# Optimization experiments

Measured on AMD Instinct MI355X. Metric: run time of the kernel, lower is better.

Reference implementation:

```python
import jax, jax.numpy as jnp
import numpy as np

EPS = 1e-7
N_INST = 16  # instance ids 1..16 (id 0 = background); all present w.h.p. given input distribution


def setup_inputs() -> dict:
    key = jax.random.key(0)
    k1, k2, k3 = jax.random.split(key, 3)
    pred_instance_mask = jax.random.uniform(k1, (4, 17, 768, 768), dtype=jnp.float32)
    cls_out = jax.random.uniform(k2, (4, 1, 768, 768), dtype=jnp.float32)
    target_mask = jax.random.randint(k3, (4, 1, 768, 768), 0, 17, dtype=jnp.int32)
    return {"pred_instance_mask": pred_instance_mask, "cls_out": cls_out, "target_mask": target_mask}


def _bce_dice(p, t):
    # BCEDiceLoss(activation=None): mean BCE on probabilities + soft-dice loss
    pc = jnp.clip(p, EPS, 1.0 - EPS)
    bce = -jnp.mean(t * jnp.log(pc) + (1.0 - t) * jnp.log1p(-pc))
    inter = jnp.sum(p * t)
    dice = 1.0 - (2.0 * inter + EPS) / (jnp.sum(p) + jnp.sum(t) + EPS)
    return bce + dice


def reference(pred_instance_mask, cls_out, target_mask):
    B, K, H, W = pred_instance_mask.shape
    tfg = (target_mask > 0).astype(jnp.float32)
    res = _bce_dice(cls_out, tfg)
    res = res + _bce_dice(pred_instance_mask[:, 0:1], 1.0 - tfg)

    # ---- pairwise BCEDice loss matrix L[n, k] for ids n=1..N_INST, channels k=1..K-1 ----
    # Each pairwise loss is over the FULL tensor (all B*H*W pixels), target = (target_mask == n).
    Pm = pred_instance_mask[:, 1:].transpose(1, 0, 2, 3).reshape(K - 1, -1)  # [K-1, M]
    Mpix = Pm.shape[1]
    tm = target_mask.reshape(-1)  # [M] int ids
    pc = jnp.clip(Pm, EPS, 1.0 - EPS)
    log1mp = jnp.log1p(-pc)
    D = log1mp - jnp.log(pc)  # [K-1, M]; BCE = mean(-log1mp) + mean(t * D)
    A = -jnp.mean(log1mp, axis=1)  # [K-1]
    segD = jax.ops.segment_sum(D.T, tm, num_segments=N_INST + 1)[1:]   # [N, K-1]
    segP = jax.ops.segment_sum(Pm.T, tm, num_segments=N_INST + 1)[1:]  # [N, K-1] = inter
    cnt = jax.ops.segment_sum(jnp.ones_like(tm, dtype=jnp.float32), tm, num_segments=N_INST + 1)[1:]  # [N]
    sum_p = jnp.sum(Pm, axis=1)  # [K-1]
    bce = A[None, :] + segD / jnp.float32(Mpix)
    dice = 1.0 - (2.0 * segP + EPS) / (sum_p[None, :] + cnt[:, None] + EPS)
    L = bce + dice  # [N, K-1]

    # ---- greedy assignment: ids in ascending order each grab the remaining best channel ----
    def step(carry, Ln):
        avail, total = carry
        masked = jnp.where(avail, Ln, jnp.inf)
        k = jnp.argmin(masked)
        return (avail.at[k].set(False), total + masked[k]), None

    (_, total), _ = jax.lax.scan(step, (jnp.ones(K - 1, dtype=bool), jnp.float32(0.0)), L)
    return (res + total) / N_INST
```

## Files before the change

### kernel.cpp

```cpp
#include <hip/hip_runtime.h>
#include <hip/hip_bf16.h>

#define HWPX 589824
#define MPIX 2359296
#define EPSF 1e-7f
#define LN2F 0.6931471805599453f
#define PXB  2304
#define NBLK 1024
#define MSTEPS 9


typedef __attribute__((ext_vector_type(8))) short bf16x8;
typedef __attribute__((ext_vector_type(4))) float f32x4;

__device__ __forceinline__ short bfc(float x) {
    union { __hip_bfloat16 h; short s; } u;
    u.h = __float2bfloat16(x);
    return u.s;
}

__device__ __forceinline__ float wave_sum64(float v) {
#pragma unroll
    for (int o = 32; o; o >>= 1) v += __shfl_xor(v, o, 64);
    return v;
}

__global__ __launch_bounds__(512, 8) void loss_main(
    const float* __restrict__ pred, const float* __restrict__ cls,
    const int* __restrict__ tm, float* __restrict__ acc)
{
    __shared__ float sD[8][256];
    __shared__ float sP[8][256];
    __shared__ float sCh[3][16][8];
    __shared__ float sC6[6][8];

    const int tid  = threadIdx.x;
    const int w    = tid >> 6;
    const int lane = tid & 63;
    const int g    = lane >> 4;
    const int q    = lane & 15;

    const long base = (long)blockIdx.x * PXB;
    const int b   = (int)(base / HWPX);
    const int off = (int)(base % HWPX);

    const int*   trow = tm   + (long)b * HWPX + off;
    const float* prow = pred + ((long)b * 17 + 1 + q) * (long)HWPX + off;

    f32x4 aD = {0.f, 0.f, 0.f, 0.f};
    f32x4 aP = {0.f, 0.f, 0.f, 0.f};
    float sl2 = 0.f, sp = 0.f, cf = 0.f;
    const int tgt = q + 1;
    const int lbase = w * 32 + g * 8;

#pragma unroll
    for (int s = 0; s < MSTEPS; ++s) {
        const int pxl = lbase + s * 256;
        const float4 pa = *(const float4*)(prow + pxl);
        const float4 pb = *(const float4*)(prow + pxl + 4);
        const int4   ta = *(const int4*)(trow + pxl);
        const int4   tb = *(const int4*)(trow + pxl + 4);
        const float pv[8] = {pa.x,pa.y,pa.z,pa.w,pb.x,pb.y,pb.z,pb.w};
        const int   tv[8] = {ta.x,ta.y,ta.z,ta.w,tb.x,tb.y,tb.z,tb.w};
        bf16x8 av, bD, bP;
#pragma unroll
        for (int j = 0; j < 8; ++j) {
            const float p  = pv[j];
            const float pc = fminf(fmaxf(p, EPSF), 1.0f - EPSF);
            const float l2p  = __log2f(pc);
            const float l21p = __log2f(1.0f - pc);
            sl2 += l21p;
            sp  += p;
            bD[j] = bfc(l21p - l2p);
            bP[j] = bfc(p);
            const bool m = (tv[j] == tgt);
            av[j] = m ? (short)0x3F80 : (short)0;
            cf += m ? 1.f : 0.f;
        }
        aD = __builtin_amdgcn_mfma_f32_16x16x32_bf16(av, bD, aD, 0, 0, 0);
        aP = __builtin_amdgcn_mfma_f32_16x16x32_bf16(av, bP, aP, 0, 0, 0);
    }

    sl2 += __shfl_xor(sl2, 16, 64); sl2 += __shfl_xor(sl2, 32, 64);
    sp  += __shfl_xor(sp,  16, 64); sp  += __shfl_xor(sp,  32, 64);
    cf  += __shfl_xor(cf,  16, 64); cf  += __shfl_xor(cf,  32, 64);
    if (lane < 16) { sCh[0][q][w] = sl2; sCh[1][q][w] = sp; sCh[2][q][w] = cf; }

    *(f32x4*)&sD[w][lane * 4] = aD;
    *(f32x4*)&sP[w][lane * 4] = aP;

    const float* crow = cls  + (long)b * HWPX + off;
    const float* zrow = pred + (long)b * 17 * (long)HWPX + off;
    float s0c=0.f,s1c=0.f,s2c=0.f, s00=0.f,s10=0.f,s20=0.f;
    const int nch = (tid < 64) ? 2 : 1;
    for (int chunk = 0; chunk < nch; ++chunk) {
        const int pbase = (chunk == 0) ? tid * 4 : 2048 + tid * 4;
        const float4 ca = *(const float4*)(crow + pbase);
        const float4 za = *(const float4*)(zrow + pbase);
        const int4   ua = *(const int4*)(trow + pbase);
        const float cv[4] = {ca.x,ca.y,ca.z,ca.w};
        const float zv[4] = {za.x,za.y,za.z,za.w};
        const int   uv[4] = {ua.x,ua.y,ua.z,ua.w};
#pragma unroll
        for (int j = 0; j < 4; ++j) {
            const int t = uv[j];
            { const float p = cv[j];
              const float pc = fminf(fmaxf(p, EPSF), 1.0f - EPSF);
              const float lp = __log2f(pc), l1p = __log2f(1.0f - pc);
              const bool fg = (t > 0);
              s0c += fg ? lp : l1p; s1c += fg ? p : 0.f; s2c += p; }
            { const float p = zv[j];
              const float pc = fminf(fmaxf(p, EPSF), 1.0f - EPSF);
              const float lp = __log2f(pc), l1p = __log2f(1.0f - pc);
              const bool bg = (t == 0);
              s00 += bg ? lp : l1p; s10 += bg ? p : 0.f; s20 += p; }
        }
    }
    s0c = wave_sum64(s0c); s1c = wave_sum64(s1c); s2c = wave_sum64(s2c);
    s00 = wave_sum64(s00); s10 = wave_sum64(s10); s20 = wave_sum64(s20);
    if (lane == 0) {
        sC6[0][w]=s0c; sC6[1][w]=s1c; sC6[2][w]=s2c;
        sC6[3][w]=s00; sC6[4][w]=s10; sC6[5][w]=s20;
    }
    __syncthreads();

    if (tid < 256) {
        const int n = tid >> 4, k = tid & 15;
        const int idx = ((((n >> 2) << 4) | k) << 2) | (n & 3);
        float dsum = 0.f, psum = 0.f;
#pragma unroll
        for (int ww = 0; ww < 8; ++ww) { dsum += sD[ww][idx]; psum += sP[ww][idx]; }
        atomicAdd(&acc[38 + n * 16 + k], dsum);
        atomicAdd(&acc[294 + n * 16 + k], psum);
    } else if (tid < 304) {
        const int i = tid - 256, qq = i >> 4, ii = i & 15;
        float t = 0.f;
#pragma unroll
        for (int ww = 0; ww < 8; ++ww) t += sCh[qq][ii][ww];
        atomicAdd(&acc[(qq == 0) ? (6 + ii) : (qq == 1) ? (22 + ii) : (550 + ii)], t);
    } else if (tid < 310) {
        const int i = tid - 304;
        float t = 0.f;
#pragma unroll
        for (int ww = 0; ww < 8; ++ww) t += sC6[i][ww];
        atomicAdd(&acc[i], t);
    }
}

__global__ void loss_final(const float* __restrict__ acc, float* __restrict__ out)
{
    __shared__ float L[16][16];
    __shared__ float s_fg;
    const int tid = threadIdx.x;
    const float Mf = (float)MPIX;

    if (tid == 0) {
        float s = 0.f;
        for (int n = 0; n < 16; ++n) s += acc[550 + n];
        s_fg = s;
    }
    __syncthreads();

    if (tid < 256) {
        const int n = tid >> 4, k = tid & 15;
        const float segD = acc[38 + n * 16 + k];
        const float segP = acc[294 + n * 16 + k];
        const float sump = acc[22 + k];
        const float cn   = acc[550 + n];
        const float bce  = (segD - acc[6 + k]) * LN2F / Mf;
        const float dice = 1.f - (2.f * segP + EPSF) / (sump + cn + EPSF);
        L[n][k] = bce + dice;
    }
    __syncthreads();

    if (tid < 64) {
        const bool mine = (tid < 16);
        float total = 0.f;
        unsigned avail = mine ? 1u : 0u;
        for (int step = 0; step < 16; ++step) {
            float v = (mine && avail) ? L[step][tid] : 1e30f;
            int idx = tid;
            #pragma unroll
            for (int o = 8; o; o >>= 1) {
                const float ov = __shfl_xor(v, o, 64);
                const int   oi = __shfl_xor(idx, o, 64);
                if (ov < v || (ov == v && oi < idx)) { v = ov; idx = oi; }
            }
            if (tid == 0) total += v;
            if (tid == idx) avail = 0;
        }
        if (tid == 0) {
            const float cnt0 = Mf - s_fg;
            const float bce_c  = -acc[0] * LN2F / Mf;
            const float dice_c = 1.f - (2.f * acc[1] + EPSF) / (acc[2] + s_fg + EPSF);
            const float bce_0  = -acc[3] * LN2F / Mf;
            const float dice_0 = 1.f - (2.f * acc[4] + EPSF) / (acc[5] + cnt0 + EPSF);
            const float res = bce_c + dice_c + bce_0 + dice_0;
            out[0] = (res + total) / 16.f;
        }
    }
}

extern "C" void kernel_launch(void* const* d_in, const int* in_sizes, int n_in,
                              void* d_out, int out_size, void* d_ws, size_t ws_size,
                              hipStream_t stream)
{
    const float* pred = (const float*)d_in[0];
    const float* cls  = (const float*)d_in[1];
    const int*   tmi  = (const int*)d_in[2];
    float* acc = (float*)d_ws;

    hipMemsetAsync(d_ws, 0, 566 * sizeof(float), stream);

    loss_main<<<dim3(NBLK), 512, 0, stream>>>(pred, cls, tmi, acc);
    loss_final<<<1, 256, 0, stream>>>(acc, (float*)d_out);
}
```

Baseline: 69.64 us.

## Stage main loop loads through LDS with async global_load_lds double buffering

Replaces direct global vector loads in the MFMA segment-sum loop with global_load_lds into a per-wave double-buffered LDS staging area, prefetching two steps ahead under explicit waitcnt control. Block size grows to 3072 pixels (768 blocks, launch bound 6 waves/SIMD), and the per-wave MFMA tile reduction moves from a strided shared array plus sum loop to LDS atomics into a single 256-entry accumulator. The aim is to overlap memory latency with the log and MFMA work and cut block count and global atomics. In exchange it adds LDS atomic contention, hand-tuned vmcnt counts that must match the issued loads, and redundant reloads at the loop tail.

```diff
diff --git a/kernel.cpp b/kernel.cpp
--- a/kernel.cpp
+++ b/kernel.cpp
@@ -5,9 +5,9 @@
 #define MPIX 2359296
 #define EPSF 1e-7f
 #define LN2F 0.6931471805599453f
-#define PXB  2304
-#define NBLK 1024
-#define MSTEPS 9
+#define MSTEPS 12
+#define PXB  3072
+#define NBLK 768
 
 
 typedef __attribute__((ext_vector_type(8))) short bf16x8;
@@ -25,14 +25,22 @@
     return v;
 }
 
-__global__ __launch_bounds__(512, 8) void loss_main(
+#define GLD16(gsrc, ldst) __builtin_amdgcn_global_load_lds( \
+    (const __attribute__((address_space(1))) void*)(gsrc),  \
+    (__attribute__((address_space(3))) void*)(ldst), 16, 0, 0)
+#define GLD4(gsrc, ldst) __builtin_amdgcn_global_load_lds(  \
+    (const __attribute__((address_space(1))) void*)(gsrc),  \
+    (__attribute__((address_space(3))) void*)(ldst), 4, 0, 0)
+
+__global__ __launch_bounds__(512, 6) void loss_main(
     const float* __restrict__ pred, const float* __restrict__ cls,
     const int* __restrict__ tm, float* __restrict__ acc)
 {
-    __shared__ float sD[8][256];
-    __shared__ float sP[8][256];
-    __shared__ float sCh[3][16][8];
-    __shared__ float sC6[6][8];
+    __shared__ float4 stP[8][2][128];
+    __shared__ int4   stT[8][2][16];
+    __shared__ float  gD[256], gP[256];
+    __shared__ float  sCh[3][16][8];
+    __shared__ float  sC6[6][8];
 
     const int tid  = threadIdx.x;
     const int w    = tid >> 6;
@@ -47,19 +55,38 @@
     const int*   trow = tm   + (long)b * HWPX + off;
     const float* prow = pred + ((long)b * 17 + 1 + q) * (long)HWPX + off;
 
+    if (tid < 256) { gD[tid] = 0.f; gP[tid] = 0.f; }
+    __syncthreads();
+
+#define STAGE(sg, buf) do {                                          \
+        const int _px = w * 32 + (sg) * 256;                         \
+        GLD16(prow + _px + g * 8,     &stP[w][buf][0]);              \
+        GLD16(prow + _px + g * 8 + 4, &stP[w][buf][64]);             \
+        GLD4 (trow + _px + (lane & 31), &stT[w][buf][0]);            \
+    } while (0)
+
+    STAGE(0, 0);
+    STAGE(1, 1);
+
     f32x4 aD = {0.f, 0.f, 0.f, 0.f};
     f32x4 aP = {0.f, 0.f, 0.f, 0.f};
     float sl2 = 0.f, sp = 0.f, cf = 0.f;
     const int tgt = q + 1;
-    const int lbase = w * 32 + g * 8;
 
 #pragma unroll
     for (int s = 0; s < MSTEPS; ++s) {
-        const int pxl = lbase + s * 256;
-        const float4 pa = *(const float4*)(prow + pxl);
-        const float4 pb = *(const float4*)(prow + pxl + 4);
-        const int4   ta = *(const int4*)(trow + pxl);
-        const int4   tb = *(const int4*)(trow + pxl + 4);
+        const int bi = s & 1;
+        asm volatile("s_waitcnt vmcnt(3)" ::: "memory");
+        __builtin_amdgcn_sched_barrier(0);
+        const float4 pa = *(const float4*)&stP[w][bi][lane];
+        const float4 pb = *(const float4*)&stP[w][bi][64 + lane];
+        const int4   ta = stT[w][bi][g * 2];
+        const int4   tb = stT[w][bi][g * 2 + 1];
+        asm volatile("s_waitcnt lgkmcnt(0)" ::: "memory");
+        __builtin_amdgcn_sched_barrier(0);
+        const int sg = (s + 2 < MSTEPS) ? s + 2 : MSTEPS - 1;
+        STAGE(sg, bi);
+
         const float pv[8] = {pa.x,pa.y,pa.z,pa.w,pb.x,pb.y,pb.z,pb.w};
         const int   tv[8] = {ta.x,ta.y,ta.z,ta.w,tb.x,tb.y,tb.z,tb.w};
         bf16x8 av, bD, bP;
@@ -80,19 +107,24 @@
         aD = __builtin_amdgcn_mfma_f32_16x16x32_bf16(av, bD, aD, 0, 0, 0);
         aP = __builtin_amdgcn_mfma_f32_16x16x32_bf16(av, bP, aP, 0, 0, 0);
     }
+#undef STAGE
 
     sl2 += __shfl_xor(sl2, 16, 64); sl2 += __shfl_xor(sl2, 32, 64);
     sp  += __shfl_xor(sp,  16, 64); sp  += __shfl_xor(sp,  32, 64);
     cf  += __shfl_xor(cf,  16, 64); cf  += __shfl_xor(cf,  32, 64);
     if (lane < 16) { sCh[0][q][w] = sl2; sCh[1][q][w] = sp; sCh[2][q][w] = cf; }
 
-    *(f32x4*)&sD[w][lane * 4] = aD;
-    *(f32x4*)&sP[w][lane * 4] = aP;
+#pragma unroll
+    for (int r = 0; r < 4; ++r) {
+        const int n = ((lane >> 4) << 2) + r;
+        atomicAdd(&gD[n * 16 + q], aD[r]);
+        atomicAdd(&gP[n * 16 + q], aP[r]);
+    }
 
     const float* crow = cls  + (long)b * HWPX + off;
     const float* zrow = pred + (long)b * 17 * (long)HWPX + off;
     float s0c=0.f,s1c=0.f,s2c=0.f, s00=0.f,s10=0.f,s20=0.f;
-    const int nch = (tid < 64) ? 2 : 1;
+    const int nch = (tid < 256) ? 2 : 1;
     for (int chunk = 0; chunk < nch; ++chunk) {
         const int pbase = (chunk == 0) ? tid * 4 : 2048 + tid * 4;
         const float4 ca = *(const float4*)(crow + pbase);
@@ -125,13 +157,8 @@
     __syncthreads();
 
     if (tid < 256) {
-        const int n = tid >> 4, k = tid & 15;
-        const int idx = ((((n >> 2) << 4) | k) << 2) | (n & 3);
-        float dsum = 0.f, psum = 0.f;
-#pragma unroll
-        for (int ww = 0; ww < 8; ++ww) { dsum += sD[ww][idx]; psum += sP[ww][idx]; }
-        atomicAdd(&acc[38 + n * 16 + k], dsum);
-        atomicAdd(&acc[294 + n * 16 + k], psum);
+        atomicAdd(&acc[38 + tid], gD[tid]);
+        atomicAdd(&acc[294 + tid], gP[tid]);
     } else if (tid < 304) {
         const int i = tid - 256, qq = i >> 4, ii = i & 15;
         float t = 0.f;
```

Result: slower. 71.05 us (+2.0%).

## Stage prediction and target tiles through LDS with double-buffered async global loads

Applied to the files above, without the earlier changes.

The main loop now copies each 256-pixel tile of the 16 instance channels and the target ids into shared memory with global_load_lds, using two buffers so the next tile's load overlaps compute on the current one. Lanes read from LDS through an XOR-swizzled layout instead of issuing strided per-lane global loads. The per-wave MFMA accumulators are combined with LDS atomics in place of a staged cross-wave reduction. In exchange the loop gains two barriers per tile and is no longer unrolled, and it relies on manual vmcnt waits that must match the number of loads issued.

```diff
diff --git a/kernel.cpp b/kernel.cpp
--- a/kernel.cpp
+++ b/kernel.cpp
@@ -5,9 +5,9 @@
 #define MPIX 2359296
 #define EPSF 1e-7f
 #define LN2F 0.6931471805599453f
+#define TILES 9
 #define PXB  2304
 #define NBLK 1024
-#define MSTEPS 9
 
 
 typedef __attribute__((ext_vector_type(8))) short bf16x8;
@@ -25,12 +25,19 @@
     return v;
 }
 
+#define GLD16(gsrc, ldst) __builtin_amdgcn_global_load_lds( \
+    (const __attribute__((address_space(1))) void*)(gsrc),  \
+    (__attribute__((address_space(3))) void*)(ldst), 16, 0, 0)
+
+#define WAITV(n) asm volatile("s_waitcnt vmcnt(" #n ")" ::: "memory")
+
 __global__ __launch_bounds__(512, 8) void loss_main(
     const float* __restrict__ pred, const float* __restrict__ cls,
     const int* __restrict__ tm, float* __restrict__ acc)
 {
-    __shared__ float sD[8][256];
-    __shared__ float sP[8][256];
+    __shared__ float stage[2][16][256];
+    __shared__ int   tmt[2][256];
+    __shared__ float gD[256], gP[256];
     __shared__ float sCh[3][16][8];
     __shared__ float sC6[6][8];
 
@@ -44,22 +51,45 @@
     const int b   = (int)(base / HWPX);
     const int off = (int)(base % HWPX);
 
-    const int*   trow = tm   + (long)b * HWPX + off;
-    const float* prow = pred + ((long)b * 17 + 1 + q) * (long)HWPX + off;
+    const int* trow = tm + (long)b * HWPX + off;
+    const float* pbase17 = pred + (long)b * 17 * (long)HWPX + off;
+
+    if (tid < 256) { gD[tid] = 0.f; gP[tid] = 0.f; }
+
+#define STAGE(t_, buf_) do {                                                      \
+        const int _r0 = w, _r1 = w + 8;                                           \
+        GLD16(pbase17 + (long)(1 + _r0) * HWPX + (t_) * 256 + ((lane ^ (_r0 & 7)) << 2), \
+              &stage[buf_][_r0][0]);                                              \
+        GLD16(pbase17 + (long)(1 + _r1) * HWPX + (t_) * 256 + ((lane ^ (_r1 & 7)) << 2), \
+              &stage[buf_][_r1][0]);                                              \
+        if (w == 0) GLD16(trow + (t_) * 256 + (lane << 2), &tmt[buf_][0]);        \
+    } while (0)
+
+    STAGE(0, 0);
 
     f32x4 aD = {0.f, 0.f, 0.f, 0.f};
     f32x4 aP = {0.f, 0.f, 0.f, 0.f};
     float sl2 = 0.f, sp = 0.f, cf = 0.f;
     const int tgt = q + 1;
-    const int lbase = w * 32 + g * 8;
-
-#pragma unroll
-    for (int s = 0; s < MSTEPS; ++s) {
-        const int pxl = lbase + s * 256;
-        const float4 pa = *(const float4*)(prow + pxl);
-        const float4 pb = *(const float4*)(prow + pxl + 4);
-        const int4   ta = *(const int4*)(trow + pxl);
-        const int4   tb = *(const int4*)(trow + pxl + 4);
+    const int s4 = w * 8 + g * 2;
+    const int k8 = q & 7;
+
+#pragma unroll 1
+    for (int t = 0; t < TILES; ++t) {
+        const int bi = t & 1;
+        if (t + 1 < TILES) {
+            STAGE(t + 1, bi ^ 1);
+            if (w == 0) WAITV(3); else WAITV(2);
+        } else {
+            WAITV(0);
+        }
+        __syncthreads();
+
+        const float4 pa = ((const float4*)&stage[bi][q][0])[s4 ^ k8];
+        const float4 pb = ((const float4*)&stage[bi][q][0])[(s4 + 1) ^ k8];
+        const int4   ta = ((const int4*)&tmt[bi][0])[s4];
+        const int4   tb = ((const int4*)&tmt[bi][0])[s4 + 1];
+
         const float pv[8] = {pa.x,pa.y,pa.z,pa.w,pb.x,pb.y,pb.z,pb.w};
         const int   tv[8] = {ta.x,ta.y,ta.z,ta.w,tb.x,tb.y,tb.z,tb.w};
         bf16x8 av, bD, bP;
@@ -79,25 +109,31 @@
         }
         aD = __builtin_amdgcn_mfma_f32_16x16x32_bf16(av, bD, aD, 0, 0, 0);
         aP = __builtin_amdgcn_mfma_f32_16x16x32_bf16(av, bP, aP, 0, 0, 0);
-    }
+        __syncthreads();
+    }
+#undef STAGE
 
     sl2 += __shfl_xor(sl2, 16, 64); sl2 += __shfl_xor(sl2, 32, 64);
     sp  += __shfl_xor(sp,  16, 64); sp  += __shfl_xor(sp,  32, 64);
     cf  += __shfl_xor(cf,  16, 64); cf  += __shfl_xor(cf,  32, 64);
     if (lane < 16) { sCh[0][q][w] = sl2; sCh[1][q][w] = sp; sCh[2][q][w] = cf; }
 
-    *(f32x4*)&sD[w][lane * 4] = aD;
-    *(f32x4*)&sP[w][lane * 4] = aP;
-
-    const float* crow = cls  + (long)b * HWPX + off;
-    const float* zrow = pred + (long)b * 17 * (long)HWPX + off;
+#pragma unroll
+    for (int r = 0; r < 4; ++r) {
+        const int n = ((lane >> 4) << 2) + r;
+        atomicAdd(&gD[n * 16 + q], aD[r]);
+        atomicAdd(&gP[n * 16 + q], aP[r]);
+    }
+
+    const float* crow = cls + (long)b * HWPX + off;
+    const float* zrow = pbase17;
     float s0c=0.f,s1c=0.f,s2c=0.f, s00=0.f,s10=0.f,s20=0.f;
     const int nch = (tid < 64) ? 2 : 1;
     for (int chunk = 0; chunk < nch; ++chunk) {
-        const int pbase = (chunk == 0) ? tid * 4 : 2048 + tid * 4;
-        const float4 ca = *(const float4*)(crow + pbase);
-        const float4 za = *(const float4*)(zrow + pbase);
-        const int4   ua = *(const int4*)(trow + pbase);
+        const int pb2 = (chunk == 0) ? tid * 4 : 2048 + tid * 4;
+        const float4 ca = *(const float4*)(crow + pb2);
+        const float4 za = *(const float4*)(zrow + pb2);
+        const int4   ua = *(const int4*)(trow + pb2);
         const float cv[4] = {ca.x,ca.y,ca.z,ca.w};
         const float zv[4] = {za.x,za.y,za.z,za.w};
         const int   uv[4] = {ua.x,ua.y,ua.z,ua.w};
@@ -125,13 +161,8 @@
     __syncthreads();
 
     if (tid < 256) {
-        const int n = tid >> 4, k = tid & 15;
-        const int idx = ((((n >> 2) << 4) | k) << 2) | (n & 3);
-        float dsum = 0.f, psum = 0.f;
-#pragma unroll
-        for (int ww = 0; ww < 8; ++ww) { dsum += sD[ww][idx]; psum += sP[ww][idx]; }
-        atomicAdd(&acc[38 + n * 16 + k], dsum);
-        atomicAdd(&acc[294 + n * 16 + k], psum);
+        atomicAdd(&acc[38 + tid], gD[tid]);
+        atomicAdd(&acc[294 + tid], gP[tid]);
     } else if (tid < 304) {
         const int i = tid - 256, qq = i >> 4, ii = i & 15;
         float t = 0.f;
```

After: 80.84 us. 16.1% more time.
